# Kernel optimization log

Measured on AMD Instinct MI355X. Metric: run time of the kernel, lower is better.

## Reference

```python
import jax, jax.numpy as jnp
import numpy as np

B, T, S, H = 4, 128, 512, 512


def setup_inputs() -> dict:
    key = jax.random.key(0)
    k1, k2, k3, k4, k5, k6, k7 = jax.random.split(key, 7)
    query = jax.random.normal(k1, (B, T, H), dtype=jnp.float32)
    encoder_outputs = jax.random.normal(k2, (B, S, H), dtype=jnp.float32)
    src_lengths = jax.random.randint(k3, (B,), 1, S + 1)
    src_lengths = src_lengths.at[0].set(S)  # torch code assumes max(len) == S
    scale = 1.0 / np.sqrt(H)
    W_h = jax.random.normal(k4, (H, H), dtype=jnp.float32) * scale
    W_s = jax.random.normal(k5, (H, H), dtype=jnp.float32) * scale
    v = jax.random.normal(k6, (H,), dtype=jnp.float32) * scale
    W_out = jax.random.normal(k7, (2 * H, H), dtype=jnp.float32) * scale
    return {"query": query, "encoder_outputs": encoder_outputs,
            "src_lengths": src_lengths, "W_h": W_h, "W_s": W_s,
            "v": v, "W_out": W_out}


def reference(query, encoder_outputs, src_lengths, W_h, W_s, v, W_out):
    # Project once, then broadcast (same math as torch's Linear on expanded tensors)
    pq = jnp.einsum('bth,hk->btk', query, W_s)            # (B,T,H) : W_s applied to query
    pe = jnp.einsum('bsh,hk->bsk', encoder_outputs, W_h)  # (B,S,H) : W_h applied to encoder
    # score(h_i, s_j) = v^T tanh(W_s q + W_h e)
    score = jnp.einsum('btsh,h->bts', jnp.tanh(pq[:, :, None, :] + pe[:, None, :, :]), v)  # (B,T,S)
    mask = (jnp.arange(score.shape[-1]) [None, :] < src_lengths[:, None])[:, None, :]  # (B,1,S)
    score = jnp.where(mask, score, -jnp.inf)
    alignment = jax.nn.softmax(score, axis=-1)            # (B,T,S)
    context = jnp.einsum('bts,bsh->bth', alignment, encoder_outputs)  # (B,T,H)
    attn_out = jnp.tanh(jnp.concatenate([context, query], axis=-1) @ W_out)  # (B,T,H)
    return attn_out
```

## Files before the change

kernel.cpp:

```cpp
#include <hip/hip_runtime.h>
#include <math.h>

#define HD 512
#define BB 4
#define TT 128
#define SS 512

typedef __attribute__((ext_vector_type(8))) short short8;
typedef __attribute__((ext_vector_type(4))) float floatx4;
typedef _Float16 half2_t __attribute__((ext_vector_type(2)));
typedef unsigned short ushort_t;
typedef unsigned int uint_t;

__device__ __forceinline__ float tanh_e(float x) {
    float t = __builtin_amdgcn_rcpf(__expf(2.f * x) + 1.f);
    return fmaf(-2.f, t, 1.f);
}
__device__ __forceinline__ ushort_t f2bf(float x) {
    unsigned int u = __float_as_uint(x);
    u += 0x7fffu + ((u >> 16) & 1u);
    return (ushort_t)(u >> 16);
}

__global__ __launch_bounds__(256) void wtrans_kernel(
    const float* __restrict__ Ws, const float* __restrict__ Wh,
    const float* __restrict__ Wo, const float* __restrict__ query,
    const float* __restrict__ enc,
    ushort_t* __restrict__ Ts, ushort_t* __restrict__ Th, ushort_t* __restrict__ To,
    ushort_t* __restrict__ cq, ushort_t* __restrict__ encB)
{
    const int bid = blockIdx.x;
    const int tid = threadIdx.x;
    if (bid < 128) {
        const float* src; ushort_t* dst; int K, l;
        if (bid < 32)      { src = Ws; dst = Ts; K = 512;  l = bid;      }
        else if (bid < 64) { src = Wh; dst = Th; K = 512;  l = bid - 32; }
        else               { src = Wo; dst = To; K = 1024; l = bid - 64; }
        const int ktiles = K >> 7;
        const int tk = l & (ktiles - 1), tn = l / ktiles;
        const int k0 = tk * 128, n0 = tn * 64;

        __shared__ ushort_t tile[64][136];

        const int lr  = tid >> 4;
        const int lc4 = (tid & 15) * 4;
        #pragma unroll
        for (int p = 0; p < 8; ++p) {
            const int row = p * 16 + lr;
            float4 s = *(const float4*)(src + (size_t)(k0 + row) * HD + n0 + lc4);
            tile[lc4 + 0][row] = f2bf(s.x);
            tile[lc4 + 1][row] = f2bf(s.y);
            tile[lc4 + 2][row] = f2bf(s.z);
            tile[lc4 + 3][row] = f2bf(s.w);
        }
        __syncthreads();
        const int n = tid >> 2, kc = (tid & 3) * 32;
        #pragma unroll
        for (int j = 0; j < 4; ++j) {
            uint4 o = *(const uint4*)&tile[n][kc + j * 8];
            *(uint4*)&dst[(size_t)(n0 + n) * K + k0 + kc + j * 8] = o;
        }
    } else if (bid < 256) {
        const int idx = ((bid - 128) * 256 + tid) * 8;
        const int m = idx >> 9, h = idx & 511;
        float4 q0 = *(const float4*)(query + (size_t)m * HD + h);
        float4 q1 = *(const float4*)(query + (size_t)m * HD + h + 4);
        uint4 o;
        o.x = (uint_t)f2bf(q0.x) | ((uint_t)f2bf(q0.y) << 16);
        o.y = (uint_t)f2bf(q0.z) | ((uint_t)f2bf(q0.w) << 16);
        o.z = (uint_t)f2bf(q1.x) | ((uint_t)f2bf(q1.y) << 16);
        o.w = (uint_t)f2bf(q1.z) | ((uint_t)f2bf(q1.w) << 16);
        *(uint4*)&cq[(size_t)m * 1024 + 512 + h] = o;
    } else {
        const size_t idx = ((size_t)(bid - 256) * 256 + tid) * 8;
        float4 e0 = *(const float4*)(enc + idx);
        float4 e1 = *(const float4*)(enc + idx + 4);
        uint4 o;
        o.x = (uint_t)f2bf(e0.x) | ((uint_t)f2bf(e0.y) << 16);
        o.y = (uint_t)f2bf(e0.z) | ((uint_t)f2bf(e0.w) << 16);
        o.z = (uint_t)f2bf(e1.x) | ((uint_t)f2bf(e1.y) << 16);
        o.w = (uint_t)f2bf(e1.z) | ((uint_t)f2bf(e1.w) << 16);
        *(uint4*)&encB[idx] = o;
    }
}

#define LDP 40
__global__ __launch_bounds__(256) void proj_kernel(
    const ushort_t* __restrict__ cq, const ushort_t* __restrict__ encB,
    const ushort_t* __restrict__ WTs, const ushort_t* __restrict__ WTh,
    const ushort_t* __restrict__ WTo, const float* __restrict__ v,
    float2* __restrict__ tqa, _Float16* __restrict__ peT,
    _Float16* __restrict__ encWo, float* __restrict__ qWob)
{
    const int bm = blockIdx.x;
    const int bn = blockIdx.y;
    int type; const ushort_t* A; int lda; const ushort_t* B; int ldb; int m0;
    if (bm < 8)       { type = 0; A = cq + 512; lda = 1024; B = WTs;       ldb = 512;  m0 = bm * 64;        }
    else if (bm < 40) { type = 1; A = encB;     lda = 512;  B = WTh;       ldb = 512;  m0 = (bm - 8) * 64;  }
    else if (bm < 72) { type = 2; A = encB;     lda = 512;  B = WTo;       ldb = 1024; m0 = (bm - 40) * 64; }
    else              { type = 3; A = cq + 512; lda = 1024; B = WTo + 512; ldb = 1024; m0 = (bm - 72) * 64; }
    const int n0 = bn * 64;

    __shared__ ushort_t As[64 * LDP];
    __shared__ ushort_t Bs[64 * LDP];

    const int tid = threadIdx.x;
    const int lane = tid & 63, w = tid >> 6;
    const int quad = lane >> 4, lrow = lane & 15;
    const int mw = (w & 1) * 32, nw = (w >> 1) * 32;

    const int ar = tid >> 2;
    const int ac = (tid & 3) * 8;

    floatx4 zero = {0.f, 0.f, 0.f, 0.f};
    floatx4 acc[2][2] = {{zero, zero}, {zero, zero}};

    uint4 ald = *(const uint4*)&A[(size_t)(m0 + ar) * lda + ac];
    uint4 bld = *(const uint4*)&B[(size_t)(n0 + ar) * ldb + ac];

    for (int k0 = 0; k0 < HD; k0 += 32) {
        __syncthreads();
        *(uint4*)&As[ar * LDP + ac] = ald;
        *(uint4*)&Bs[ar * LDP + ac] = bld;
        __syncthreads();
        if (k0 + 32 < HD) {
            ald = *(const uint4*)&A[(size_t)(m0 + ar) * lda + k0 + 32 + ac];
            bld = *(const uint4*)&B[(size_t)(n0 + ar) * ldb + k0 + 32 + ac];
        }
        short8 af[2], bf[2];
        #pragma unroll
        for (int i = 0; i < 2; ++i)
            af[i] = *(const short8*)&As[(mw + i * 16 + lrow) * LDP + quad * 8];
        #pragma unroll
        for (int j = 0; j < 2; ++j)
            bf[j] = *(const short8*)&Bs[(nw + j * 16 + lrow) * LDP + quad * 8];
        #pragma unroll
        for (int i = 0; i < 2; ++i)
            #pragma unroll
            for (int j = 0; j < 2; ++j)
                acc[i][j] = __builtin_amdgcn_mfma_f32_16x16x32_bf16(af[i], bf[j], acc[i][j], 0, 0, 0);
    }

    if (type == 0) {
        #pragma unroll
        for (int j = 0; j < 2; ++j) {
            const int col = n0 + nw + j * 16 + lrow;
            const float vj = v[col];
            #pragma unroll
            for (int i = 0; i < 2; ++i)
                #pragma unroll
                for (int r = 0; r < 4; ++r) {
                    const int row = m0 + mw + i * 16 + quad * 4 + r;
                    float tq = tanh_e(acc[i][j][r]);
                    float2 o; o.x = tq; o.y = vj * tq;
                    tqa[(size_t)row * HD + col] = o;
                }
        }
    } else if (type == 1) {
        #pragma unroll
        for (int i = 0; i < 2; ++i)
            #pragma unroll
            for (int j = 0; j < 2; ++j) {
                const int gm = m0 + mw + i * 16 + quad * 4;
                const int b = gm >> 9, s = gm & 511;
                const int col = n0 + nw + j * 16 + lrow;
                _Float16 t0 = (_Float16)tanh_e(acc[i][j][0]);
                _Float16 t1 = (_Float16)tanh_e(acc[i][j][1]);
                _Float16 t2 = (_Float16)tanh_e(acc[i][j][2]);
                _Float16 t3 = (_Float16)tanh_e(acc[i][j][3]);
                ushort4 o;
                o.x = *(ushort_t*)&t0; o.y = *(ushort_t*)&t1;
                o.z = *(ushort_t*)&t2; o.w = *(ushort_t*)&t3;
                *(ushort4*)((ushort_t*)peT + ((size_t)b * HD + col) * SS + s) = o;
            }
    } else if (type == 2) {
        #pragma unroll
        for (int i = 0; i < 2; ++i)
            #pragma unroll
            for (int j = 0; j < 2; ++j) {
                const int col = n0 + nw + j * 16 + lrow;
                #pragma unroll
                for (int r = 0; r < 4; ++r) {
                    const int gm = m0 + mw + i * 16 + quad * 4 + r;
                    encWo[(size_t)gm * HD + col] = (_Float16)acc[i][j][r];
                }
            }
    } else {
        #pragma unroll
        for (int i = 0; i < 2; ++i)
            #pragma unroll
            for (int j = 0; j < 2; ++j) {
                const int col = n0 + nw + j * 16 + lrow;
                #pragma unroll
                for (int r = 0; r < 4; ++r) {
                    const int gm = m0 + mw + i * 16 + quad * 4 + r;
                    qWob[(size_t)gm * HD + col] = acc[i][j][r];
                }
            }
    }
}

__global__ __launch_bounds__(512) void fused_kernel(
    const float2* __restrict__ tqa, const _Float16* __restrict__ peT,
    const float* __restrict__ vv, const _Float16* __restrict__ encWo,
    const float* __restrict__ qWob, const int* __restrict__ lens,
    float* __restrict__ out)
{
    const int bt = blockIdx.x;
    const int b = bt >> 7;
    const int tid = threadIdx.x;
    const int lane = tid & 63, wid = tid >> 6;
    const int hh = tid >> 8;
    const int si = (tid & 255) * 2;
    const int len = lens[b];

    __shared__ uint4  s_tab[HD];
    __shared__ float  s_sc[SS];
    __shared__ uint_t s_al2[SS];
    __shared__ float  s_red[16];

    {
        float2 q = tqa[(size_t)bt * HD + tid];
        float vh = vv[tid];
        _Float16 tqh = (_Float16)q.x, vvh = (_Float16)vh, vth = (_Float16)q.y;
        uint_t ta = *(ushort_t*)&tqh, tb = *(ushort_t*)&vvh, tc = *(ushort_t*)&vth;
        uint4 e; e.x = ta | (ta << 16); e.y = tb | (tb << 16); e.z = tc | (tc << 16); e.w = 0;
        s_tab[tid] = e;
    }
    __syncthreads();

    float acc0 = 0.f, acc1 = 0.f;
    if (si < len) {
        const ushort_t* colp = (const ushort_t*)peT + (size_t)b * HD * SS
                             + (size_t)(hh * 256) * SS + si;
        const uint4* tabp = &s_tab[hh * 256];
        half2_t one2; one2[0] = (_Float16)1.f; one2[1] = (_Float16)1.f;
        #pragma unroll 4
        for (int hp = 0; hp < 128; ++hp) {
            uint_t pA = *(const uint_t*)(colp + (size_t)(2 * hp) * SS);
            uint_t pB = *(const uint_t*)(colp + (size_t)(2 * hp + 1) * SS);
            uint4 cA = tabp[2 * hp], cB = tabp[2 * hp + 1];
            half2_t teA = *(half2_t*)&pA, teB = *(half2_t*)&pB;
            half2_t tqA = *(half2_t*)&cA.x, vA = *(half2_t*)&cA.y, vtA = *(half2_t*)&cA.z;
            half2_t tqB = *(half2_t*)&cB.x, vB = *(half2_t*)&cB.y, vtB = *(half2_t*)&cB.z;
            half2_t dA = tqA * teA + one2;
            half2_t dB = tqB * teB + one2;
            half2_t mA = vA * teA + vtA;
            half2_t mB = vB * teB + vtB;
            half2_t num = mA * dB + mB * dA;
            half2_t den = dA * dB;
            float nf0 = (float)num[0], nf1 = (float)num[1];
            float df0 = (float)den[0], df1 = (float)den[1];
            acc0 = fmaf(nf0, __builtin_amdgcn_rcpf(df0), acc0);
            acc1 = fmaf(nf1, __builtin_amdgcn_rcpf(df1), acc1);
        }
    }
    if (hh) { s_sc[si] = acc0; s_sc[si + 1] = acc1; }
    __syncthreads();
    if (!hh) {
        float t0 = acc0 + s_sc[si], t1 = acc1 + s_sc[si + 1];
        s_sc[si]     = (si     < len) ? t0 : -INFINITY;
        s_sc[si + 1] = (si + 1 < len) ? t1 : -INFINITY;
    }
    __syncthreads();

    float sc = s_sc[tid];
    float m = sc;
    #pragma unroll
    for (int off = 32; off; off >>= 1) m = fmaxf(m, __shfl_xor(m, off, 64));
    if (lane == 0) s_red[wid] = m;
    __syncthreads();
    m = s_red[0];
    #pragma unroll
    for (int i2 = 1; i2 < 8; ++i2) m = fmaxf(m, s_red[i2]);

    float e = __expf(sc - m);
    float sum = e;
    #pragma unroll
    for (int off = 32; off; off >>= 1) sum += __shfl_xor(sum, off, 64);
    if (lane == 0) s_red[8 + wid] = sum;
    __syncthreads();
    float total = s_red[8];
    #pragma unroll
    for (int i2 = 1; i2 < 8; ++i2) total += s_red[8 + i2];
    {
        float a = e * __builtin_amdgcn_rcpf(total);
        _Float16 ah = (_Float16)a;
        uint_t ap = *(ushort_t*)&ah;
        s_al2[tid] = ap | (ap << 16);
    }
    __syncthreads();

    const int n0 = si;
    float o0 = 0.f, o1 = 0.f;
    const ushort_t* ew = (const ushort_t*)encWo + (size_t)b * SS * HD + n0;
    const int sbeg = hh * 256;
    const int send = (sbeg + 256 < len) ? sbeg + 256 : len;
    int s = sbeg;
    for (; s + 16 <= send; s += 16) {
        half2_t acch; acch[0] = (_Float16)0.f; acch[1] = (_Float16)0.f;
        #pragma unroll
        for (int k = 0; k < 16; ++k) {
            uint_t wv = *(const uint_t*)(ew + (size_t)(s + k) * HD);
            uint_t av = s_al2[s + k];
            half2_t eh = *(half2_t*)&wv, a2 = *(half2_t*)&av;
            acch = a2 * eh + acch;
        }
        o0 += (float)acch[0]; o1 += (float)acch[1];
    }
    for (; s < send; ++s) {
        uint_t wv = *(const uint_t*)(ew + (size_t)s * HD);
        half2_t eh = *(half2_t*)&wv;
        uint_t av = s_al2[s];
        _Float16 ah16 = *(_Float16*)&av;
        float a = (float)ah16;
        o0 = fmaf(a, (float)eh[0], o0);
        o1 = fmaf(a, (float)eh[1], o1);
    }
    if (hh) { s_sc[n0] = o0; s_sc[n0 + 1] = o1; }
    __syncthreads();
    if (!hh) {
        float2 qb = *(const float2*)(qWob + (size_t)bt * HD + n0);
        float f0 = o0 + s_sc[n0] + qb.x;
        float f1 = o1 + s_sc[n0 + 1] + qb.y;
        float2 ov; ov.x = tanh_e(f0); ov.y = tanh_e(f1);
        *(float2*)(out + (size_t)bt * HD + n0) = ov;
    }
}

extern "C" void kernel_launch(void* const* d_in, const int* in_sizes, int n_in,
                              void* d_out, int out_size, void* d_ws, size_t ws_size,
                              hipStream_t stream) {
    (void)in_sizes; (void)n_in; (void)out_size; (void)ws_size;
    const float* query = (const float*)d_in[0];
    const float* enc   = (const float*)d_in[1];
    const int*   lens  = (const int*)d_in[2];
    const float* W_h   = (const float*)d_in[3];
    const float* W_s   = (const float*)d_in[4];
    const float* v     = (const float*)d_in[5];
    const float* W_out = (const float*)d_in[6];
    float* out = (float*)d_out;

    ushort_t* WTs   = (ushort_t*)d_ws;
    ushort_t* WTh   = WTs + (size_t)HD * HD;
    ushort_t* WTo   = WTh + (size_t)HD * HD;
    ushort_t* encB  = WTo + (size_t)HD * 2 * HD;
    float2*   tqa   = (float2*)(encB + (size_t)BB * SS * HD);
    _Float16* peT   = (_Float16*)(tqa + (size_t)BB * TT * HD);
    _Float16* encWo = peT + (size_t)BB * HD * SS;
    float*    qWob  = (float*)(encWo + (size_t)BB * SS * HD);
    ushort_t* cq    = (ushort_t*)(qWob + (size_t)BB * TT * HD);

    wtrans_kernel<<<dim3(768), 256, 0, stream>>>(W_s, W_h, W_out, query, enc,
                                                 WTs, WTh, WTo, cq, encB);
    proj_kernel<<<dim3(80, 8), 256, 0, stream>>>(cq, encB, WTs, WTh, WTo, v,
                                                 tqa, peT, encWo, qWob);
    fused_kernel<<<dim3(BB * TT), 512, 0, stream>>>(tqa, peT, v, encWo, qWob, lens, out);
}
```

Measured before the change: 118.6 us.

## Widen fused attention kernel to 1024 threads with 8-way split reductions

The fused score/softmax/context kernel now launches 1024 threads per block instead of 512. Each thread handles 4 source positions (or 4 output columns) over one eighth of the hidden (or source) dimension. Partial sums are combined through a new 7x512 shared-memory buffer. Loads are widened to 64-bit to cover the extra columns, and softmax reductions now span 16 waves. The aim is more parallelism and memory-level parallelism per (b,t) row, at the cost of more shared memory, extra reduction passes and possible register pressure under the 1024-thread bound.

```diff
diff --git a/kernel.cpp b/kernel.cpp
--- a/kernel.cpp
+++ b/kernel.cpp
@@ -200,7 +200,7 @@
     }
 }
 
-__global__ __launch_bounds__(512) void fused_kernel(
+__global__ __launch_bounds__(1024, 8) void fused_kernel(
     const float2* __restrict__ tqa, const _Float16* __restrict__ peT,
     const float* __restrict__ vv, const _Float16* __restrict__ encWo,
     const float* __restrict__ qWob, const int* __restrict__ lens,
@@ -210,61 +210,75 @@
     const int b = bt >> 7;
     const int tid = threadIdx.x;
     const int lane = tid & 63, wid = tid >> 6;
-    const int hh = tid >> 8;
-    const int si = (tid & 255) * 2;
     const int len = lens[b];
 
     __shared__ uint4  s_tab[HD];
+    __shared__ float  s_part[7 * SS];
     __shared__ float  s_sc[SS];
     __shared__ uint_t s_al2[SS];
-    __shared__ float  s_red[16];
-
-    {
+    __shared__ float  s_red[32];
+
+    if (tid < HD) {
         float2 q = tqa[(size_t)bt * HD + tid];
         float vh = vv[tid];
         _Float16 tqh = (_Float16)q.x, vvh = (_Float16)vh, vth = (_Float16)q.y;
         uint_t ta = *(ushort_t*)&tqh, tb = *(ushort_t*)&vvh, tc = *(ushort_t*)&vth;
-        uint4 e; e.x = ta | (ta << 16); e.y = tb | (tb << 16); e.z = tc | (tc << 16); e.w = 0;
-        s_tab[tid] = e;
-    }
-    __syncthreads();
-
-    float acc0 = 0.f, acc1 = 0.f;
-    if (si < len) {
-        const ushort_t* colp = (const ushort_t*)peT + (size_t)b * HD * SS
-                             + (size_t)(hh * 256) * SS + si;
-        const uint4* tabp = &s_tab[hh * 256];
+        uint4 e4; e4.x = ta | (ta << 16); e4.y = tb | (tb << 16); e4.z = tc | (tc << 16); e4.w = 0;
+        s_tab[tid] = e4;
+    }
+    __syncthreads();
+
+    const int sg = tid & 127, hq = tid >> 7;
+    const int s0 = sg * 4;
+    const int hbase = hq * 64;
+    float a0 = 0.f, a1 = 0.f, a2 = 0.f, a3 = 0.f;
+    if (s0 < len) {
+        const ushort_t* colp = (const ushort_t*)peT + ((size_t)b * HD + hbase) * SS + s0;
+        const uint4* tabp = &s_tab[hbase];
         half2_t one2; one2[0] = (_Float16)1.f; one2[1] = (_Float16)1.f;
-        #pragma unroll 4
-        for (int hp = 0; hp < 128; ++hp) {
-            uint_t pA = *(const uint_t*)(colp + (size_t)(2 * hp) * SS);
-            uint_t pB = *(const uint_t*)(colp + (size_t)(2 * hp + 1) * SS);
-            uint4 cA = tabp[2 * hp], cB = tabp[2 * hp + 1];
-            half2_t teA = *(half2_t*)&pA, teB = *(half2_t*)&pB;
+        #pragma unroll 2
+        for (int i = 0; i < 32; ++i) {
+            uint2 pA = *(const uint2*)(colp);
+            uint2 pB = *(const uint2*)(colp + SS);
+            colp += 2 * SS;
+            uint4 cA = tabp[2 * i], cB = tabp[2 * i + 1];
             half2_t tqA = *(half2_t*)&cA.x, vA = *(half2_t*)&cA.y, vtA = *(half2_t*)&cA.z;
             half2_t tqB = *(half2_t*)&cB.x, vB = *(half2_t*)&cB.y, vtB = *(half2_t*)&cB.z;
-            half2_t dA = tqA * teA + one2;
-            half2_t dB = tqB * teB + one2;
-            half2_t mA = vA * teA + vtA;
-            half2_t mB = vB * teB + vtB;
-            half2_t num = mA * dB + mB * dA;
-            half2_t den = dA * dB;
-            float nf0 = (float)num[0], nf1 = (float)num[1];
-            float df0 = (float)den[0], df1 = (float)den[1];
-            acc0 = fmaf(nf0, __builtin_amdgcn_rcpf(df0), acc0);
-            acc1 = fmaf(nf1, __builtin_amdgcn_rcpf(df1), acc1);
-        }
-    }
-    if (hh) { s_sc[si] = acc0; s_sc[si + 1] = acc1; }
-    __syncthreads();
-    if (!hh) {
-        float t0 = acc0 + s_sc[si], t1 = acc1 + s_sc[si + 1];
-        s_sc[si]     = (si     < len) ? t0 : -INFINITY;
-        s_sc[si + 1] = (si + 1 < len) ? t1 : -INFINITY;
-    }
-    __syncthreads();
-
-    float sc = s_sc[tid];
+            half2_t teA01 = *(half2_t*)&pA.x, teA23 = *(half2_t*)&pA.y;
+            half2_t teB01 = *(half2_t*)&pB.x, teB23 = *(half2_t*)&pB.y;
+            half2_t dA01 = tqA * teA01 + one2, dA23 = tqA * teA23 + one2;
+            half2_t dB01 = tqB * teB01 + one2, dB23 = tqB * teB23 + one2;
+            half2_t mA01 = vA * teA01 + vtA,  mA23 = vA * teA23 + vtA;
+            half2_t mB01 = vB * teB01 + vtB,  mB23 = vB * teB23 + vtB;
+            half2_t n01 = mA01 * dB01 + mB01 * dA01;
+            half2_t n23 = mA23 * dB23 + mB23 * dA23;
+            half2_t d01 = dA01 * dB01, d23 = dA23 * dB23;
+            a0 = fmaf((float)n01[0], __builtin_amdgcn_rcpf((float)d01[0]), a0);
+            a1 = fmaf((float)n01[1], __builtin_amdgcn_rcpf((float)d01[1]), a1);
+            a2 = fmaf((float)n23[0], __builtin_amdgcn_rcpf((float)d23[0]), a2);
+            a3 = fmaf((float)n23[1], __builtin_amdgcn_rcpf((float)d23[1]), a3);
+        }
+    }
+    if (hq) {
+        float4 p; p.x = a0; p.y = a1; p.z = a2; p.w = a3;
+        *(float4*)&s_part[(hq - 1) * SS + s0] = p;
+    }
+    __syncthreads();
+    if (!hq) {
+        float t0 = a0, t1 = a1, t2 = a2, t3 = a3;
+        #pragma unroll
+        for (int q = 0; q < 7; ++q) {
+            float4 p = *(const float4*)&s_part[q * SS + s0];
+            t0 += p.x; t1 += p.y; t2 += p.z; t3 += p.w;
+        }
+        s_sc[s0]     = (s0     < len) ? t0 : -INFINITY;
+        s_sc[s0 + 1] = (s0 + 1 < len) ? t1 : -INFINITY;
+        s_sc[s0 + 2] = (s0 + 2 < len) ? t2 : -INFINITY;
+        s_sc[s0 + 3] = (s0 + 3 < len) ? t3 : -INFINITY;
+    }
+    __syncthreads();
+
+    float sc = (tid < SS) ? s_sc[tid] : -INFINITY;
     float m = sc;
     #pragma unroll
     for (int off = 32; off; off >>= 1) m = fmaxf(m, __shfl_xor(m, off, 64));
@@ -272,18 +286,18 @@
     __syncthreads();
     m = s_red[0];
     #pragma unroll
-    for (int i2 = 1; i2 < 8; ++i2) m = fmaxf(m, s_red[i2]);
-
-    float e = __expf(sc - m);
+    for (int i2 = 1; i2 < 16; ++i2) m = fmaxf(m, s_red[i2]);
+
+    float e = (tid < SS) ? __expf(sc - m) : 0.f;
     float sum = e;
     #pragma unroll
     for (int off = 32; off; off >>= 1) sum += __shfl_xor(sum, off, 64);
-    if (lane == 0) s_red[8 + wid] = sum;
-    __syncthreads();
-    float total = s_red[8];
+    if (lane == 0) s_red[16 + wid] = sum;
+    __syncthreads();
+    float total = s_red[16];
     #pragma unroll
-    for (int i2 = 1; i2 < 8; ++i2) total += s_red[8 + i2];
-    {
+    for (int i2 = 1; i2 < 16; ++i2) total += s_red[16 + i2];
+    if (tid < SS) {
         float a = e * __builtin_amdgcn_rcpf(total);
         _Float16 ah = (_Float16)a;
         uint_t ap = *(ushort_t*)&ah;
@@ -291,40 +305,46 @@
     }
     __syncthreads();
 
-    const int n0 = si;
-    float o0 = 0.f, o1 = 0.f;
-    const ushort_t* ew = (const ushort_t*)encWo + (size_t)b * SS * HD + n0;
-    const int sbeg = hh * 256;
-    const int send = (sbeg + 256 < len) ? sbeg + 256 : len;
-    int s = sbeg;
-    for (; s + 16 <= send; s += 16) {
-        half2_t acch; acch[0] = (_Float16)0.f; acch[1] = (_Float16)0.f;
-        #pragma unroll
-        for (int k = 0; k < 16; ++k) {
-            uint_t wv = *(const uint_t*)(ew + (size_t)(s + k) * HD);
-            uint_t av = s_al2[s + k];
-            half2_t eh = *(half2_t*)&wv, a2 = *(half2_t*)&av;
-            acch = a2 * eh + acch;
-        }
-        o0 += (float)acch[0]; o1 += (float)acch[1];
-    }
-    for (; s < send; ++s) {
-        uint_t wv = *(const uint_t*)(ew + (size_t)s * HD);
-        half2_t eh = *(half2_t*)&wv;
-        uint_t av = s_al2[s];
-        _Float16 ah16 = *(_Float16*)&av;
-        float a = (float)ah16;
-        o0 = fmaf(a, (float)eh[0], o0);
-        o1 = fmaf(a, (float)eh[1], o1);
-    }
-    if (hh) { s_sc[n0] = o0; s_sc[n0 + 1] = o1; }
-    __syncthreads();
-    if (!hh) {
-        float2 qb = *(const float2*)(qWob + (size_t)bt * HD + n0);
-        float f0 = o0 + s_sc[n0] + qb.x;
-        float f1 = o1 + s_sc[n0 + 1] + qb.y;
-        float2 ov; ov.x = tanh_e(f0); ov.y = tanh_e(f1);
-        *(float2*)(out + (size_t)bt * HD + n0) = ov;
+    const int ng = tid & 127, sq = tid >> 7;
+    const int n0 = ng * 4;
+    const int sbeg = sq * 64;
+    float o0 = 0.f, o1 = 0.f, o2 = 0.f, o3 = 0.f;
+    {
+        const ushort_t* ew = (const ushort_t*)encWo + ((size_t)b * SS + sbeg) * HD + n0;
+        const int rem = (len > sbeg) ? ((len - sbeg < 64) ? len - sbeg : 64) : 0;
+        const int schunks = (rem + 7) >> 3;
+        for (int c = 0; c < schunks; ++c) {
+            half2_t acc01; acc01[0] = (_Float16)0.f; acc01[1] = (_Float16)0.f;
+            half2_t acc23; acc23[0] = (_Float16)0.f; acc23[1] = (_Float16)0.f;
+            const ushort_t* ewc = ew + (size_t)(c * 8) * HD;
+            #pragma unroll
+            for (int k = 0; k < 8; ++k) {
+                uint2 wv = *(const uint2*)(ewc + (size_t)k * HD);
+                uint_t av = s_al2[sbeg + c * 8 + k];
+                half2_t a2h = *(half2_t*)&av;
+                acc01 = a2h * (*(half2_t*)&wv.x) + acc01;
+                acc23 = a2h * (*(half2_t*)&wv.y) + acc23;
+            }
+            o0 += (float)acc01[0]; o1 += (float)acc01[1];
+            o2 += (float)acc23[0]; o3 += (float)acc23[1];
+        }
+    }
+    if (sq) {
+        float4 p; p.x = o0; p.y = o1; p.z = o2; p.w = o3;
+        *(float4*)&s_part[(sq - 1) * SS + n0] = p;
+    }
+    __syncthreads();
+    if (!sq) {
+        #pragma unroll
+        for (int q = 0; q < 7; ++q) {
+            float4 p = *(const float4*)&s_part[q * SS + n0];
+            o0 += p.x; o1 += p.y; o2 += p.z; o3 += p.w;
+        }
+        float4 qb = *(const float4*)(qWob + (size_t)bt * HD + n0);
+        float4 ov;
+        ov.x = tanh_e(o0 + qb.x); ov.y = tanh_e(o1 + qb.y);
+        ov.z = tanh_e(o2 + qb.z); ov.w = tanh_e(o3 + qb.w);
+        *(float4*)(out + (size_t)bt * HD + n0) = ov;
     }
 }
 
@@ -355,5 +375,5 @@
                                                  WTs, WTh, WTo, cq, encB);
     proj_kernel<<<dim3(80, 8), 256, 0, stream>>>(cq, encB, WTs, WTh, WTo, v,
                                                  tqa, peT, encWo, qWob);
-    fused_kernel<<<dim3(BB * TT), 512, 0, stream>>>(tqa, peT, v, encWo, qWob, lens, out);
-}
+    fused_kernel<<<dim3(BB * TT), 1024, 0, stream>>>(tqa, peT, v, encWo, qWob, lens, out);
+}
```

Result: no change. 118.2 us (-0.4%).
